# Kernel tuning notes

Measured on AMD Instinct MI355X. Metric: run time of the kernel, lower is better.

## Reference

```python
import jax, jax.numpy as jnp
import numpy as np

N = 100000
E = 3200000
H = 4        # heads
C = 8        # hidden_dim per head
G = 512      # number of graphs
F_IN = 128
NEG_SLOPE = 0.2


def glorot(key, shape):
    fan = shape[0] + shape[-1]
    lim = jnp.sqrt(6.0 / fan)
    return jax.random.uniform(key, shape, jnp.float32, -lim, lim)


def setup_inputs() -> dict:
    key = jax.random.key(0)
    ks = jax.random.split(key, 32)
    x = jax.random.normal(ks[0], (N, F_IN), jnp.float32)
    edge_index = jax.random.randint(ks[1], (2, E), 0, N, jnp.int64)
    batch = jnp.sort(jax.random.randint(ks[2], (N,), 0, G, jnp.int64))
    d = {"x": x, "edge_index": edge_index, "batch": batch}
    in_dims = [F_IN, H * C, H * C, H * C]
    for i, din in enumerate(in_dims, start=1):
        d[f"W{i}"] = glorot(ks[3 + 4 * i], (din, H * C))
        d[f"as{i}"] = glorot(ks[4 + 4 * i], (H, C))
        d[f"ad{i}"] = glorot(ks[5 + 4 * i], (H, C))
        d[f"b{i}"] = jnp.zeros((H * C,), jnp.float32)
    d["fc_w"] = glorot(ks[30], (H * C, 1))
    d["fc_b"] = jnp.zeros((1,), jnp.float32)
    return d


def gat_layer(x, src, dst, W, a_src, a_dst, b):
    # x: [N, din]; src/dst: [E'] (with self-loops); returns [N, H*C]
    h = (x @ W).reshape(N, H, C)                         # [N,H,C]
    al_s = jnp.einsum('nhc,hc->nh', h, a_src)            # [N,H]
    al_d = jnp.einsum('nhc,hc->nh', h, a_dst)
    e = jax.nn.leaky_relu(al_s[src] + al_d[dst], NEG_SLOPE)  # [E',H]
    m = jax.ops.segment_max(e, dst, num_segments=N)      # [N,H]
    ee = jnp.exp(e - m[dst])
    denom = jax.ops.segment_sum(ee, dst, num_segments=N) # [N,H]
    alpha = ee / denom[dst]
    msg = alpha[:, :, None] * h[src]                     # [E',H,C]
    out = jax.ops.segment_sum(msg, dst, num_segments=N)  # [N,H,C]
    return out.reshape(N, H * C) + b


def reference(x, edge_index, batch, W1, as1, ad1, b1, W2, as2, ad2, b2,
              W3, as3, ad3, b3, W4, as4, ad4, b4, fc_w, fc_b):
    # PyG GATConv default: add self-loops
    loop = jnp.arange(N, dtype=edge_index.dtype)
    src = jnp.concatenate([edge_index[0], loop])
    dst = jnp.concatenate([edge_index[1], loop])
    h = jax.nn.elu(gat_layer(x, src, dst, W1, as1, ad1, b1))
    h = jax.nn.elu(gat_layer(h, src, dst, W2, as2, ad2, b2))
    h = jax.nn.elu(gat_layer(h, src, dst, W3, as3, ad3, b3))
    h = jax.nn.elu(gat_layer(h, src, dst, W4, as4, ad4, b4))
    # global mean pool over graphs
    sums = jax.ops.segment_sum(h, batch, num_segments=G)          # [G,HC]
    cnts = jax.ops.segment_sum(jnp.ones((N,), h.dtype), batch, num_segments=G)
    pooled = sums / jnp.maximum(cnts, 1.0)[:, None]
    return pooled @ fc_w + fc_b                                   # [G,1]
```

## Files before the change

### kernel.cpp

```cpp
#include <hip/hip_runtime.h>
#include <hip/hip_fp16.h>
#include <math.h>

#define NN 100000
#define NE 3200000
#define NHEAD 4
#define HC 32
#define NG 512
#define EDGES (NE + NN)

#define G1BLKS (NN / 8)

#define BKT_BITS 9
#define BKT_SIZE 512
#define NBKT 196
#define CHUNK1 16384
#define NB1 ((EDGES + CHUNK1 - 1) / CHUNK1)
#define NB1S 204
#define CAP2 18432
#define PCHUNK 128

__device__ __forceinline__ float lrelu(float x) { return x > 0.f ? x : 0.2f * x; }

__global__ __launch_bounds__(256) void gemm1(
    const float* __restrict__ x, const float* __restrict__ W1,
    const float* __restrict__ as1, const float* __restrict__ ad1,
    __half* __restrict__ h, float* __restrict__ als, float* __restrict__ ald) {
    __shared__ float Wl[128 * HC];
    __shared__ float xl[8][128];
    int tid = threadIdx.x;
    for (int i = tid; i < 128 * HC; i += 256) Wl[i] = W1[i];
    int n0 = blockIdx.x * 8;
    {
        float4 v = *reinterpret_cast<const float4*>(x + n0 * 128 + tid * 4);
        int idx = tid * 4;
        int r = idx >> 7, c = idx & 127;
        *reinterpret_cast<float4*>(&xl[r][c]) = v;
    }
    __syncthreads();
    int r = tid >> 5, col = tid & 31;
    int n = n0 + r;
    float acc = 0.f;
#pragma unroll
    for (int k = 0; k < 128; ++k) acc = fmaf(xl[r][k], Wl[k * HC + col], acc);
    float s = acc * as1[col];
    float d = acc * ad1[col];
#pragma unroll
    for (int off = 1; off < 8; off <<= 1) {
        s += __shfl_xor(s, off);
        d += __shfl_xor(d, off);
    }
    h[n * HC + col] = __float2half(acc);
    if ((col & 7) == 0) {
        als[n * NHEAD + (col >> 3)] = s;
        ald[n * NHEAD + (col >> 3)] = d;
    }
}

__global__ __launch_bounds__(512) void pass1_hist(const int* __restrict__ ei,
                                                  int* __restrict__ CmatT) {
    __shared__ int hcnt[NBKT];
    for (int i = threadIdx.x; i < NBKT; i += 512) hcnt[i] = 0;
    __syncthreads();
    int base = blockIdx.x * CHUNK1;
    int lim = min(base + CHUNK1, EDGES);
    for (int e = base + threadIdx.x; e < lim; e += 512) {
        int dst = (e < NE) ? ei[NE + e] : (e - NE);
        atomicAdd(&hcnt[dst >> BKT_BITS], 1);
    }
    __syncthreads();
    for (int i = threadIdx.x; i < NBKT; i += 512)
        CmatT[i * NB1S + blockIdx.x] = hcnt[i];
}

__global__ __launch_bounds__(64) void colscan2(int* __restrict__ CmatT,
                                               int* __restrict__ degTot) {
    int k = blockIdx.x;
    int lane = threadIdx.x;
    int* p = CmatT + k * NB1S;
    int i0 = lane * 4;
    int v0 = (i0 + 0 < NB1) ? p[i0 + 0] : 0;
    int v1 = (i0 + 1 < NB1) ? p[i0 + 1] : 0;
    int v2 = (i0 + 2 < NB1) ? p[i0 + 2] : 0;
    int v3 = (i0 + 3 < NB1) ? p[i0 + 3] : 0;
    int e1 = v0, e2 = v0 + v1, e3 = v0 + v1 + v2;
    int tot = e3 + v3;
    int run = tot;
#pragma unroll
    for (int off = 1; off < 64; off <<= 1) {
        int u = __shfl_up(run, off);
        if (lane >= off) run += u;
    }
    int excl = run - tot;
    if (i0 + 0 < NB1) p[i0 + 0] = excl;
    if (i0 + 1 < NB1) p[i0 + 1] = excl + e1;
    if (i0 + 2 < NB1) p[i0 + 2] = excl + e2;
    if (i0 + 3 < NB1) p[i0 + 3] = excl + e3;
    if (lane == 63) degTot[k] = run;
}

__global__ __launch_bounds__(256) void bucket_apex(const int* __restrict__ degTot,
                                                   int* __restrict__ bucketStart) {
    __shared__ int tot[256];
    int k = threadIdx.x;
    int own = (k < NBKT) ? degTot[k] : 0;
    tot[k] = own;
    __syncthreads();
    for (int off = 1; off < 256; off <<= 1) {
        int u = (k >= off) ? tot[k - off] : 0;
        __syncthreads();
        tot[k] += u;
        __syncthreads();
    }
    if (k < NBKT) bucketStart[k] = tot[k] - own;
    if (k == 255) bucketStart[NBKT] = tot[255];
}

__global__ __launch_bounds__(512) void pass1_scatter(const int* __restrict__ ei,
                                                     const int* __restrict__ CmatT,
                                                     const int* __restrict__ bucketStart,
                                                     unsigned int* __restrict__ ebuf) {
    __shared__ int cur[NBKT];
    for (int i = threadIdx.x; i < NBKT; i += 512)
        cur[i] = bucketStart[i] + CmatT[i * NB1S + blockIdx.x];
    __syncthreads();
    int base = blockIdx.x * CHUNK1;
    int lim = min(base + CHUNK1, EDGES);
    for (int e = base + threadIdx.x; e < lim; e += 512) {
        int src, dst;
        if (e < NE) { src = ei[e]; dst = ei[NE + e]; }
        else        { src = dst = e - NE; }
        int pos = atomicAdd(&cur[dst >> BKT_BITS], 1);
        ebuf[pos] = ((unsigned int)(dst & (BKT_SIZE - 1)) << 20) | (unsigned int)src;
    }
}

__global__ __launch_bounds__(1024) void pass2_sort(const unsigned int* __restrict__ ebuf,
                                                   const int* __restrict__ bucketStart,
                                                   int* __restrict__ csrsrc,
                                                   int* __restrict__ rowst) {
    __shared__ int hist[BKT_SIZE];
    __shared__ int scn[BKT_SIZE];
    __shared__ int staging[CAP2];
    int t = threadIdx.x;
    int k = blockIdx.x;
    int start = bucketStart[k], end = bucketStart[k + 1];
    int count = end - start;
    if (t < BKT_SIZE) hist[t] = 0;
    __syncthreads();
    for (int i = start + t; i < end; i += 1024)
        atomicAdd(&hist[ebuf[i] >> 20], 1);
    __syncthreads();
    if (t < BKT_SIZE) scn[t] = hist[t];
    __syncthreads();
    for (int off = 1; off < BKT_SIZE; off <<= 1) {
        int u = (t < BKT_SIZE && t >= off) ? scn[t - off] : 0;
        __syncthreads();
        if (t < BKT_SIZE) scn[t] += u;
        __syncthreads();
    }
    if (t < BKT_SIZE) {
        int ex = scn[t] - hist[t];
        rowst[k * BKT_SIZE + t] = start + ex;
        hist[t] = ex;
    }
    __syncthreads();
    for (int i = start + t; i < end; i += 1024) {
        unsigned int v = ebuf[i];
        int pos = atomicAdd(&hist[v >> 20], 1);
        if (pos < CAP2) staging[pos] = (int)(v & 0xFFFFFu);
    }
    __syncthreads();
    for (int i = t; i < count; i += 1024) csrsrc[start + i] = staging[i];
}

template<bool FUSE>
__global__ __launch_bounds__(256) void agg_layer(
    const int* __restrict__ rowst, const int* __restrict__ csrsrc,
    const float* __restrict__ als, const float* __restrict__ ald,
    const __half* __restrict__ h, const float* __restrict__ bias,
    const float* __restrict__ Wn, const float* __restrict__ asn,
    const float* __restrict__ adn,
    __half* __restrict__ h_out, float* __restrict__ als_out,
    float* __restrict__ ald_out, float* __restrict__ act_out) {
    __shared__ float Wl[HC * HC];
    int tid = threadIdx.x;
    if (FUSE) {
        for (int i = tid; i < HC * HC; i += 256) Wl[i] = Wn[i];
        __syncthreads();
    }
    int g = blockIdx.x * 8 + (tid >> 5);
    int lane = tid & 31;
    int head = lane >> 3;
    int slot = lane & 7;
    float adh = ald[g * NHEAD + head];
    int beg = rowst[g], end = rowst[g + 1];

    float acc[8];
#pragma unroll
    for (int j = 0; j < 8; ++j) acc[j] = 0.f;
    float dsum = 0.f;
    const __half* hL = h + lane;

    for (int c0 = beg; c0 < end; c0 += 8) {
        int e = c0 + slot;
        int s = (e < end) ? csrsrc[e] : 0;
        float p = __expf(lrelu(als[s * NHEAD + head] + adh));
        p = (e < end) ? p : 0.f;
        dsum += p;
#pragma unroll
        for (int j = 0; j < 8; ++j) {
            float pj = __shfl(p, (head << 3) | j, 32);
            int sj = __shfl(s, j, 32);
            acc[j] = fmaf(pj, __half2float(hL[sj * HC]), acc[j]);
        }
    }
    float a = ((acc[0] + acc[1]) + (acc[2] + acc[3])) +
              ((acc[4] + acc[5]) + (acc[6] + acc[7]));
    dsum += __shfl_xor(dsum, 1, 32);
    dsum += __shfl_xor(dsum, 2, 32);
    dsum += __shfl_xor(dsum, 4, 32);

    float v = a / dsum + bias[lane];
    float av = v > 0.f ? v : (__expf(v) - 1.f);
    if (!FUSE) {
        act_out[g * HC + lane] = av;
        return;
    }
    float hacc = 0.f;
#pragma unroll
    for (int kk = 0; kk < HC; ++kk)
        hacc = fmaf(__shfl(av, kk, 32), Wl[kk * HC + lane], hacc);
    h_out[g * HC + lane] = __float2half(hacc);
    float sv = hacc * asn[lane];
    float dv = hacc * adn[lane];
#pragma unroll
    for (int off = 1; off < 8; off <<= 1) {
        sv += __shfl_xor(sv, off);
        dv += __shfl_xor(dv, off);
    }
    if ((lane & 7) == 0) {
        als_out[g * NHEAD + head] = sv;
        ald_out[g * NHEAD + head] = dv;
    }
}

__global__ void pool_init(float* __restrict__ sums, float* __restrict__ cnt) {
    int i = blockIdx.x * blockDim.x + threadIdx.x;
    if (i < NG * HC) sums[i] = 0.f;
    if (i < NG) cnt[i] = 0.f;
}

__global__ __launch_bounds__(256) void pool_seg(const float* __restrict__ act,
                                                const int* __restrict__ batch,
                                                float* __restrict__ sums,
                                                float* __restrict__ cnt) {
    int grp = blockIdx.x * 8 + (threadIdx.x >> 5);
    int lane = threadIdx.x & 31;
    int n0 = grp * PCHUNK;
    if (n0 >= NN) return;
    int n1 = min(n0 + PCHUNK, NN);
    int curg = batch[n0];
    float acc = 0.f, c = 0.f;
    for (int n = n0; n < n1; ++n) {
        int gg = batch[n];
        if (gg != curg) {
            atomicAdd(&sums[curg * HC + lane], acc);
            if (lane == 0) atomicAdd(&cnt[curg], c);
            acc = 0.f; c = 0.f; curg = gg;
        }
        acc += act[n * HC + lane];
        c += 1.f;
    }
    atomicAdd(&sums[curg * HC + lane], acc);
    if (lane == 0) atomicAdd(&cnt[curg], c);
}

__global__ void fc_out(const float* __restrict__ sums, const float* __restrict__ cnt,
                       const float* __restrict__ fcw, const float* __restrict__ fcb,
                       float* __restrict__ out) {
    int g = blockIdx.x;
    int lane = threadIdx.x;
    float v = (lane < HC) ? sums[g * HC + lane] * fcw[lane] : 0.f;
#pragma unroll
    for (int off = 32; off; off >>= 1) v += __shfl_down(v, off);
    if (lane == 0) out[g] = v / fmaxf(cnt[g], 1.f) + fcb[0];
}

extern "C" void kernel_launch(void* const* d_in, const int* in_sizes, int n_in,
                              void* d_out, int out_size, void* d_ws, size_t ws_size,
                              hipStream_t stream) {
    const float* x     = (const float*)d_in[0];
    const int*   ei    = (const int*)d_in[1];
    const int*   batch = (const int*)d_in[2];
    const float* W[4]   = {(const float*)d_in[3],  (const float*)d_in[7],
                           (const float*)d_in[11], (const float*)d_in[15]};
    const float* asr[4] = {(const float*)d_in[4],  (const float*)d_in[8],
                           (const float*)d_in[12], (const float*)d_in[16]};
    const float* adt[4] = {(const float*)d_in[5],  (const float*)d_in[9],
                           (const float*)d_in[13], (const float*)d_in[17]};
    const float* bb[4]  = {(const float*)d_in[6],  (const float*)d_in[10],
                           (const float*)d_in[14], (const float*)d_in[18]};
    const float* fcw = (const float*)d_in[19];
    const float* fcb = (const float*)d_in[20];
    float* out = (float*)d_out;

    char* ws = (char*)d_ws;
    size_t off = 0;
    auto carve = [&](size_t bytes) {
        void* p = ws + off;
        off += (bytes + 255) & ~size_t(255);
        return p;
    };
    __half* hA   = (__half*)carve(sizeof(__half) * NN * HC);
    __half* hB   = (__half*)carve(sizeof(__half) * NN * HC);
    float* actF  = (float*)carve(sizeof(float) * NN * HC);
    float* alsA  = (float*)carve(sizeof(float) * NN * NHEAD);
    float* aldA  = (float*)carve(sizeof(float) * NN * NHEAD);
    float* alsB  = (float*)carve(sizeof(float) * NN * NHEAD);
    float* aldB  = (float*)carve(sizeof(float) * NN * NHEAD);
    int*   CmatT = (int*)carve(sizeof(int) * NBKT * NB1S);
    int*   degTot= (int*)carve(sizeof(int) * NBKT);
    int*   bkst  = (int*)carve(sizeof(int) * (NBKT + 1));
    unsigned int* ebuf = (unsigned int*)carve(sizeof(unsigned int) * EDGES);
    int*   rowst = (int*)carve(sizeof(int) * NBKT * BKT_SIZE);
    int*   csrsrc= (int*)carve(sizeof(int) * EDGES);
    float* sums  = (float*)carve(sizeof(float) * NG * HC);
    float* cnt   = (float*)carve(sizeof(float) * NG);

    pass1_hist<<<NB1, 512, 0, stream>>>(ei, CmatT);
    colscan2<<<NBKT, 64, 0, stream>>>(CmatT, degTot);
    bucket_apex<<<1, 256, 0, stream>>>(degTot, bkst);
    pass1_scatter<<<NB1, 512, 0, stream>>>(ei, CmatT, bkst, ebuf);
    pass2_sort<<<NBKT, 1024, 0, stream>>>(ebuf, bkst, csrsrc, rowst);

    gemm1<<<G1BLKS, 256, 0, stream>>>(x, W[0], asr[0], adt[0], hA, alsA, aldA);

    agg_layer<true><<<G1BLKS, 256, 0, stream>>>(rowst, csrsrc, alsA, aldA, hA, bb[0],
                                                W[1], asr[1], adt[1],
                                                hB, alsB, aldB, nullptr);
    agg_layer<true><<<G1BLKS, 256, 0, stream>>>(rowst, csrsrc, alsB, aldB, hB, bb[1],
                                                W[2], asr[2], adt[2],
                                                hA, alsA, aldA, nullptr);
    agg_layer<true><<<G1BLKS, 256, 0, stream>>>(rowst, csrsrc, alsA, aldA, hA, bb[2],
                                                W[3], asr[3], adt[3],
                                                hB, alsB, aldB, nullptr);
    agg_layer<false><<<G1BLKS, 256, 0, stream>>>(rowst, csrsrc, alsB, aldB, hB, bb[3],
                                                 nullptr, nullptr, nullptr,
                                                 nullptr, nullptr, nullptr, actF);

    pool_init<<<(NG * HC + 255) / 256, 256, 0, stream>>>(sums, cnt);
    pool_seg<<<((NN + PCHUNK - 1) / PCHUNK + 7) / 8, 256, 0, stream>>>(actF, batch,
                                                                       sums, cnt);
    fc_out<<<NG, 64, 0, stream>>>(sums, cnt, fcw, fcb, out);
}
```

Before: 444.6 us.

## Sort CSR neighbors by source quarter and unroll aggregation to 16 edges

The bucket sort now bins each destination's edges by source-id quarter, so neighbors within a row come out roughly ordered by source. This gives the gathers more locality. The sort replaces the 512-entry scan with a 1024-thread scan over paired bins. The aggregation loop handles 16 edges per iteration, issues all gathered half loads before the FMAs to expose memory-level parallelism, and uses nontemporal loads for csrsrc. Costs are more registers per thread and a slightly heavier sort pass.

```diff
diff --git a/kernel.cpp b/kernel.cpp
--- a/kernel.cpp
+++ b/kernel.cpp
@@ -18,9 +18,13 @@
 #define NB1 ((EDGES + CHUNK1 - 1) / CHUNK1)
 #define NB1S 204
 #define CAP2 18432
+#define NBIN2 2048
 #define PCHUNK 128
 
 __device__ __forceinline__ float lrelu(float x) { return x > 0.f ? x : 0.2f * x; }
+__device__ __forceinline__ int src_quarter(int src) {
+    return (src >= 50000) ? ((src >= 75000) ? 3 : 2) : ((src >= 25000) ? 1 : 0);
+}
 
 __global__ __launch_bounds__(256) void gemm1(
     const float* __restrict__ x, const float* __restrict__ W1,
@@ -139,36 +143,43 @@
                                                    const int* __restrict__ bucketStart,
                                                    int* __restrict__ csrsrc,
                                                    int* __restrict__ rowst) {
-    __shared__ int hist[BKT_SIZE];
-    __shared__ int scn[BKT_SIZE];
+    __shared__ int hist[NBIN2];
+    __shared__ int pairs[1024];
     __shared__ int staging[CAP2];
     int t = threadIdx.x;
     int k = blockIdx.x;
     int start = bucketStart[k], end = bucketStart[k + 1];
     int count = end - start;
-    if (t < BKT_SIZE) hist[t] = 0;
-    __syncthreads();
-    for (int i = start + t; i < end; i += 1024)
-        atomicAdd(&hist[ebuf[i] >> 20], 1);
-    __syncthreads();
-    if (t < BKT_SIZE) scn[t] = hist[t];
-    __syncthreads();
-    for (int off = 1; off < BKT_SIZE; off <<= 1) {
-        int u = (t < BKT_SIZE && t >= off) ? scn[t - off] : 0;
-        __syncthreads();
-        if (t < BKT_SIZE) scn[t] += u;
-        __syncthreads();
-    }
-    if (t < BKT_SIZE) {
-        int ex = scn[t] - hist[t];
-        rowst[k * BKT_SIZE + t] = start + ex;
-        hist[t] = ex;
-    }
+    hist[t] = 0;
+    hist[t + 1024] = 0;
     __syncthreads();
     for (int i = start + t; i < end; i += 1024) {
         unsigned int v = ebuf[i];
-        int pos = atomicAdd(&hist[v >> 20], 1);
-        if (pos < CAP2) staging[pos] = (int)(v & 0xFFFFFu);
+        int src = (int)(v & 0xFFFFFu);
+        atomicAdd(&hist[(int)((v >> 20) << 2) | src_quarter(src)], 1);
+    }
+    __syncthreads();
+    int h0 = hist[2 * t], h1 = hist[2 * t + 1];
+    pairs[t] = h0 + h1;
+    __syncthreads();
+    for (int off = 1; off < 1024; off <<= 1) {
+        int u = (t >= off) ? pairs[t - off] : 0;
+        __syncthreads();
+        pairs[t] += u;
+        __syncthreads();
+    }
+    int e0 = pairs[t] - h0 - h1;
+    int e1 = e0 + h0;
+    __syncthreads();
+    hist[2 * t] = e0;
+    hist[2 * t + 1] = e1;
+    if ((t & 1) == 0) rowst[k * BKT_SIZE + (t >> 1)] = start + e0;
+    __syncthreads();
+    for (int i = start + t; i < end; i += 1024) {
+        unsigned int v = ebuf[i];
+        int src = (int)(v & 0xFFFFFu);
+        int pos = atomicAdd(&hist[(int)((v >> 20) << 2) | src_quarter(src)], 1);
+        if (pos < CAP2) staging[pos] = src;
     }
     __syncthreads();
     for (int i = t; i < count; i += 1024) csrsrc[start + i] = staging[i];
@@ -202,18 +213,33 @@
     float dsum = 0.f;
     const __half* hL = h + lane;
 
-    for (int c0 = beg; c0 < end; c0 += 8) {
-        int e = c0 + slot;
-        int s = (e < end) ? csrsrc[e] : 0;
-        float p = __expf(lrelu(als[s * NHEAD + head] + adh));
-        p = (e < end) ? p : 0.f;
-        dsum += p;
+    for (int c0 = beg; c0 < end; c0 += 16) {
+        int eA = c0 + slot;
+        int eB = eA + 8;
+        int sA = (eA < end) ? __builtin_nontemporal_load(csrsrc + eA) : 0;
+        int sB = (eB < end) ? __builtin_nontemporal_load(csrsrc + eB) : 0;
+        float pA = __expf(lrelu(als[sA * NHEAD + head] + adh));
+        float pB = __expf(lrelu(als[sB * NHEAD + head] + adh));
+        pA = (eA < end) ? pA : 0.f;
+        pB = (eB < end) ? pB : 0.f;
+        dsum += pA + pB;
+        int sjA[8], sjB[8];
 #pragma unroll
         for (int j = 0; j < 8; ++j) {
-            float pj = __shfl(p, (head << 3) | j, 32);
-            int sj = __shfl(s, j, 32);
-            acc[j] = fmaf(pj, __half2float(hL[sj * HC]), acc[j]);
+            sjA[j] = __shfl(sA, j, 32);
+            sjB[j] = __shfl(sB, j, 32);
         }
+        __half hvA[8], hvB[8];
+#pragma unroll
+        for (int j = 0; j < 8; ++j) hvA[j] = hL[sjA[j] * HC];
+#pragma unroll
+        for (int j = 0; j < 8; ++j) hvB[j] = hL[sjB[j] * HC];
+#pragma unroll
+        for (int j = 0; j < 8; ++j)
+            acc[j] = fmaf(__shfl(pA, (head << 3) | j, 32), __half2float(hvA[j]), acc[j]);
+#pragma unroll
+        for (int j = 0; j < 8; ++j)
+            acc[j] = fmaf(__shfl(pB, (head << 3) | j, 32), __half2float(hvB[j]), acc[j]);
     }
     float a = ((acc[0] + acc[1]) + (acc[2] + acc[3])) +
               ((acc[4] + acc[5]) + (acc[6] + acc[7]));
```

Result: slower. 473.0 us (+6.4%).

## Merge gemm1 with edge histogram and prefetch next source indices in aggregation

Applied to the files above, without the earlier changes.

Fuses the layer-1 GEMM and the edge-destination histogram into one launch, with extra blocks doing the histogram, so the two independent pieces of work run concurrently and one launch is saved. In the aggregation loop it software-pipelines the csrsrc load and the source attention-logit gather for the next chunk, and uses nontemporal loads for csrsrc, to hide gather latency. Histogram blocks now use 256 threads instead of 512 and reserve the GEMM's shared memory, which may lower occupancy. The prefetch adds register pressure.

```diff
diff --git a/kernel.cpp b/kernel.cpp
--- a/kernel.cpp
+++ b/kernel.cpp
@@ -22,13 +22,30 @@
 
 __device__ __forceinline__ float lrelu(float x) { return x > 0.f ? x : 0.2f * x; }
 
-__global__ __launch_bounds__(256) void gemm1(
+__global__ __launch_bounds__(256) void gemm1_hist(
     const float* __restrict__ x, const float* __restrict__ W1,
     const float* __restrict__ as1, const float* __restrict__ ad1,
-    __half* __restrict__ h, float* __restrict__ als, float* __restrict__ ald) {
+    __half* __restrict__ h, float* __restrict__ als, float* __restrict__ ald,
+    const int* __restrict__ ei, int* __restrict__ CmatT) {
     __shared__ float Wl[128 * HC];
     __shared__ float xl[8][128];
+    __shared__ int hcnt[NBKT];
     int tid = threadIdx.x;
+    if (blockIdx.x >= G1BLKS) {
+        int b1 = blockIdx.x - G1BLKS;
+        for (int i = tid; i < NBKT; i += 256) hcnt[i] = 0;
+        __syncthreads();
+        int base = b1 * CHUNK1;
+        int lim = min(base + CHUNK1, EDGES);
+        for (int e = base + tid; e < lim; e += 256) {
+            int dst = (e < NE) ? ei[NE + e] : (e - NE);
+            atomicAdd(&hcnt[dst >> BKT_BITS], 1);
+        }
+        __syncthreads();
+        for (int i = tid; i < NBKT; i += 256)
+            CmatT[i * NB1S + b1] = hcnt[i];
+        return;
+    }
     for (int i = tid; i < 128 * HC; i += 256) Wl[i] = W1[i];
     int n0 = blockIdx.x * 8;
     {
@@ -55,22 +72,6 @@
         als[n * NHEAD + (col >> 3)] = s;
         ald[n * NHEAD + (col >> 3)] = d;
     }
-}
-
-__global__ __launch_bounds__(512) void pass1_hist(const int* __restrict__ ei,
-                                                  int* __restrict__ CmatT) {
-    __shared__ int hcnt[NBKT];
-    for (int i = threadIdx.x; i < NBKT; i += 512) hcnt[i] = 0;
-    __syncthreads();
-    int base = blockIdx.x * CHUNK1;
-    int lim = min(base + CHUNK1, EDGES);
-    for (int e = base + threadIdx.x; e < lim; e += 512) {
-        int dst = (e < NE) ? ei[NE + e] : (e - NE);
-        atomicAdd(&hcnt[dst >> BKT_BITS], 1);
-    }
-    __syncthreads();
-    for (int i = threadIdx.x; i < NBKT; i += 512)
-        CmatT[i * NB1S + blockIdx.x] = hcnt[i];
 }
 
 __global__ __launch_bounds__(64) void colscan2(int* __restrict__ CmatT,
@@ -202,18 +203,26 @@
     float dsum = 0.f;
     const __half* hL = h + lane;
 
+    int e0 = beg + slot;
+    int sP = (e0 < end) ? __builtin_nontemporal_load(csrsrc + e0) : 0;
+    float aP = als[sP * NHEAD + head];
+
     for (int c0 = beg; c0 < end; c0 += 8) {
-        int e = c0 + slot;
-        int s = (e < end) ? csrsrc[e] : 0;
-        float p = __expf(lrelu(als[s * NHEAD + head] + adh));
-        p = (e < end) ? p : 0.f;
+        int eN = c0 + 8 + slot;
+        int sN = (eN < end) ? __builtin_nontemporal_load(csrsrc + eN) : 0;
+        float aN = als[sN * NHEAD + head];
+        bool ok = (c0 + slot) < end;
+        float p = __expf(lrelu(aP + adh));
+        p = ok ? p : 0.f;
         dsum += p;
 #pragma unroll
         for (int j = 0; j < 8; ++j) {
             float pj = __shfl(p, (head << 3) | j, 32);
-            int sj = __shfl(s, j, 32);
+            int sj = __shfl(sP, j, 32);
             acc[j] = fmaf(pj, __half2float(hL[sj * HC]), acc[j]);
         }
+        sP = sN;
+        aP = aN;
     }
     float a = ((acc[0] + acc[1]) + (acc[2] + acc[3])) +
               ((acc[4] + acc[5]) + (acc[6] + acc[7]));
@@ -328,13 +337,12 @@
     float* sums  = (float*)carve(sizeof(float) * NG * HC);
     float* cnt   = (float*)carve(sizeof(float) * NG);
 
-    pass1_hist<<<NB1, 512, 0, stream>>>(ei, CmatT);
+    gemm1_hist<<<G1BLKS + NB1, 256, 0, stream>>>(x, W[0], asr[0], adt[0],
+                                                 hA, alsA, aldA, ei, CmatT);
     colscan2<<<NBKT, 64, 0, stream>>>(CmatT, degTot);
     bucket_apex<<<1, 256, 0, stream>>>(degTot, bkst);
     pass1_scatter<<<NB1, 512, 0, stream>>>(ei, CmatT, bkst, ebuf);
     pass2_sort<<<NBKT, 1024, 0, stream>>>(ebuf, bkst, csrsrc, rowst);
-
-    gemm1<<<G1BLKS, 256, 0, stream>>>(x, W[0], asr[0], adt[0], hA, alsA, aldA);
 
     agg_layer<true><<<G1BLKS, 256, 0, stream>>>(rowst, csrsrc, alsA, aldA, hA, bb[0],
                                                 W[1], asr[1], adt[1],
```

After: 461.7 us. 1.04x slower.
